# Kernel optimization log

Measured on AMD Instinct MI355X. Metric: run time of the kernel, lower is better.

Reference implementation:

```python
import jax, jax.numpy as jnp
import numpy as np

V, E, H, T, B = 10004, 96, 670, 20, 256


def setup_inputs() -> dict:
    key = jax.random.key(0)
    ks = iter(jax.random.split(key, 48))
    def p(*shape):
        return jax.random.normal(next(ks), shape, jnp.float32) * 0.05
    emb = p(V, E).at[0].set(0.0)  # padding_idx=0 row zeroed
    return dict(
        x=jax.random.randint(next(ks), (B, T), 0, V, jnp.int32),
        emb=emb,
        g_wi=p(4 * H, E), g_wh=p(4 * H, H), g_bi=p(4 * H), g_bh=p(4 * H),
        l_wi=p(4 * H, E), l_wh=p(4 * H, H), l_bi=p(4 * H), l_bh=p(4 * H),
        gl1_w=p(E, H), gl1_b=p(E), ll1_w=p(E, H), ll1_b=p(E),
        gl2_w=p(V, E), gl2_b=p(V), ll2_w=p(V, E), ll2_b=p(V),
        p1_w=p(500, E + 2 * H), p1_b=p(500),
        p2_w=p(250, 500), p2_b=p(250),
        p3_w=p(100, 250), p3_b=p(100),
        p4_w=p(50, 100), p4_b=p(50),
        pe_w=p(2, 50), pe_b=p(2),
        q1_w=p(75, 192), q1_b=p(75),
        q2_w=p(30, 75), q2_b=p(30),
        q2e_w=p(2, 30), q2e_b=p(2),
        q3_w=p(10, 30), q3_b=p(10),
        q3e_w=p(2, 10), q3e_b=p(2),
    )


def _lstm(x, h, c, wi, wh, bi, bh):
    # torch.nn.LSTMCell gate order: i, f, g, o
    g = x @ wi.T + bi + h @ wh.T + bh
    i, f, gg, o = jnp.split(g, 4, axis=-1)
    c = jax.nn.sigmoid(f) * c + jax.nn.sigmoid(i) * jnp.tanh(gg)
    h = jax.nn.sigmoid(o) * jnp.tanh(c)
    return h, c


def reference(x, emb, g_wi, g_wh, g_bi, g_bh, l_wi, l_wh, l_bi, l_bh,
              gl1_w, gl1_b, ll1_w, ll1_b, gl2_w, gl2_b, ll2_w, ll2_b,
              p1_w, p1_b, p2_w, p2_b, p3_w, p3_b, p4_w, p4_b, pe_w, pe_b,
              q1_w, q1_b, q2_w, q2_b, q2e_w, q2e_b, q3_w, q3_b, q3e_w, q3e_b):
    relu = jax.nn.relu
    embs = emb[x]                      # [B,T,E]
    Bb, Tt = x.shape
    Hh = g_wh.shape[1]
    z0 = jnp.zeros((Bb, Hh), embs.dtype)

    def step(carry, e_t):
        gh, gc, lh, lc = carry
        gh, gc = _lstm(e_t, gh, gc, g_wi, g_wh, g_bi, g_bh)
        lh, lc = _lstm(e_t, lh, lc, l_wi, l_wh, l_bi, l_bh)
        h = relu(jnp.concatenate([e_t, gh, lh], 1) @ p1_w.T + p1_b)
        h = relu(h @ p2_w.T + p2_b)
        h = relu(h @ p3_w.T + p3_b)
        h = relu(h @ p4_w.T + p4_b)
        prob = jax.nn.softmax(h @ pe_w.T + pe_b, axis=1)  # [B,2]
        # bmm([B,1,2],[B,2,H]) with tilde=[local, global]
        ghm = prob[:, 0:1] * lh + prob[:, 1:2] * gh
        gcm = prob[:, 0:1] * lc + prob[:, 1:2] * gc
        return (ghm, gcm, lh, lc), (ghm, prob)

    _, (hs, probs) = jax.lax.scan(step, (z0, z0, z0, z0), jnp.swapaxes(embs, 0, 1))
    hidden_states = jnp.swapaxes(hs, 0, 1)    # [B,T,H]
    probs_loop = jnp.swapaxes(probs, 0, 1)    # [B,T,2]

    global_x = hidden_states @ gl1_w.T + gl1_b  # [B,T,E]
    local_x = hidden_states @ ll1_w.T + ll1_b   # [B,T,E]
    sf = jnp.concatenate([global_x, local_x], -1)  # [B,T,192]
    h = relu(sf @ q1_w.T + q1_b)
    h = relu(h @ q2_w.T + q2_b)
    y = relu(h @ q2e_w.T + q2e_b)               # p1 logits [B,T,2]
    h2 = relu(h @ q3_w.T + q3_b)
    zz = relu(h2 @ q3e_w.T + q3e_b)             # p2 logits [B,T,2]

    p1s = jax.nn.softmax(y, axis=2)
    ph = jnp.broadcast_to(probs_loop[:, :, None, :], (Bb, Tt, Tt, 2))  # repeat(1,1,T,1)
    ph = jnp.concatenate([ph, p1s[:, None, :, :]], axis=1)
    xm = p1s[:, :, 0:1] * global_x + p1s[:, :, 1:2] * local_x
    gl = xm @ gl2_w.T + gl2_b                   # [B,T,V]
    ll = xm @ ll2_w.T + ll2_b
    p2s = jax.nn.softmax(zz, axis=2)
    ph = jnp.concatenate([ph, p2s[:, None, :, :]], axis=1)  # [B,T+2,T,2]
    logits = gl * p2s[:, :, 0:1] + ll * p2s[:, :, 1:2]
    return jnp.transpose(logits, (0, 2, 1)), ph
```

## Files before the change

kernel.cpp:

```cpp
#include <hip/hip_runtime.h>

#define DI __device__ __forceinline__

typedef unsigned short u16;
typedef unsigned int u32;
typedef __bf16 bf16x8 __attribute__((ext_vector_type(8)));
typedef float f32x4 __attribute__((ext_vector_type(4)));

static constexpr int B = 256, Tn = 20, En = 96, Hn = 670, Vn = 10004;
static constexpr int HP = 672;

DI float bf2f(u16 u) { union { u32 i; float f; } v; v.i = ((u32)u) << 16; return v.f; }
DI u16 f2bf(float f) {
    u32 u = __float_as_uint(f);
    u32 r = (u + 0x7FFFu + ((u >> 16) & 1u)) >> 16;
    return (u16)r;
}
DI float sigm(float x) { return 1.f / (1.f + __expf(-x)); }
DI float tanha(float x) {
    x = fminf(fmaxf(x, -15.f), 15.f);
    float e = __expf(2.f * x);
    return (e - 1.f) / (e + 1.f);
}
DI bf16x8 frag(const u16* p) { return *(const bf16x8*)p; }
DI f32x4 mfma16(bf16x8 a, bf16x8 b, f32x4 c) {
    return __builtin_amdgcn_mfma_f32_16x16x32_bf16(a, b, c, 0, 0, 0);
}
DI u16 ldw(const u16* src, long long i, int f) {
    return f ? f2bf(((const float*)src)[i]) : src[i];
}
DI float ldf(const u16* src, long long i, int f) {
    return f ? ((const float*)src)[i] : bf2f(src[i]);
}

struct Ptrs {
    const int* x;
    const u16 *emb, *g_wi, *g_wh, *g_bi, *g_bh, *l_wi, *l_wh, *l_bi, *l_bh;
    const u16 *gl1_w, *gl1_b, *ll1_w, *ll1_b, *gl2_w, *gl2_b, *ll2_w, *ll2_b;
    const u16 *p1_w, *p1_b, *p2_w, *p2_b, *p3_w, *p3_b, *p4_w, *p4_b, *pe_w, *pe_b;
    const u16 *q1_w, *q1_b, *q2_w, *q2_b, *q2e_w, *q2e_b, *q3_w, *q3_b, *q3e_w, *q3e_b;
    int  *flagp;
    u16 *embs;
    u16 *WgCat;
    u16 *P1W;
    u16 *W1C;
    u16 *W2C;
    float *BSUM;
    u16 *hs;
    u16 *hcat;
    u16 *uw;
    float *ghf, *gcf, *lhf, *lc2, *gcm;
    float *L1out;
    float *sf;
    float *p2sbuf;
    u16 *n_p1b, *n_p2w, *n_p2b, *n_p3w, *n_p3b, *n_p4w, *n_p4b, *n_pew, *n_peb;
    u16 *n_gl1b, *n_ll1b, *n_gl2b, *n_ll2b;
    u16 *n_q1w, *n_q1b, *n_q2w, *n_q2b, *n_q2ew, *n_q2eb, *n_q3w, *n_q3b, *n_q3ew, *n_q3eb;
    u16 *out0, *out1;
    float *out0f, *out1f;
};

__global__ __launch_bounds__(64) void k_detect(Ptrs p) {
    int lane = threadIdx.x;
    u32 d = ((const u32*)p.g_bi)[lane];
    u16 lo = (u16)(d & 0xffffu);
    int e = (lo >> 7) & 0xff;
    unsigned long long m = __ballot(e >= 127);
    if (lane == 0) p.flagp[0] = (m != 0ull) ? 1 : 0;
}

__global__ __launch_bounds__(256) void k_norm(Ptrs p) {
    const int f = p.flagp[0];
    int i = blockIdx.x * 256 + threadIdx.x;
    const u16* srcs[23] = {p.p1_b, p.p2_w, p.p2_b, p.p3_w, p.p3_b, p.p4_w, p.p4_b,
                           p.pe_w, p.pe_b, p.gl1_b, p.ll1_b, p.gl2_b, p.ll2_b,
                           p.q1_w, p.q1_b, p.q2_w, p.q2_b, p.q2e_w, p.q2e_b,
                           p.q3_w, p.q3_b, p.q3e_w, p.q3e_b};
    u16* dsts[23] = {p.n_p1b, p.n_p2w, p.n_p2b, p.n_p3w, p.n_p3b, p.n_p4w, p.n_p4b,
                     p.n_pew, p.n_peb, p.n_gl1b, p.n_ll1b, p.n_gl2b, p.n_ll2b,
                     p.n_q1w, p.n_q1b, p.n_q2w, p.n_q2b, p.n_q2ew, p.n_q2eb,
                     p.n_q3w, p.n_q3b, p.n_q3ew, p.n_q3eb};
    const int ns[23] = {500, 125000, 250, 25000, 100, 5000, 50, 100, 2, 96, 96, 10004, 10004,
                        14400, 75, 2250, 30, 60, 2, 300, 10, 20, 2};
    #pragma unroll 1
    for (int s = 0; s < 23; ++s) {
        if (i < ns[s]) { dsts[s][i] = ldw(srcs[s], i, f); return; }
        i -= ns[s];
    }
}

__global__ __launch_bounds__(256) void k_prep(Ptrs p) {
    const int f = p.flagp[0];
    int i = blockIdx.x * 256 + threadIdx.x;
    if (i < 491520) {
        int r = i / 96, j = i % 96;
        int t = r >> 8, b = r & 255;
        int idx = p.x[b * Tn + t];
        p.embs[r * 96 + j] = ldw(p.emb, (long long)idx * 96 + j, f);
        return;
    }
    i -= 491520;
    if (i < 2 * 2680 * 768) {
        int z = i / (2680 * 768);
        int rem = i - z * (2680 * 768);
        int col = rem / 768, k = rem % 768;
        const u16* wi = z ? p.l_wi : p.g_wi;
        const u16* wh = z ? p.l_wh : p.g_wh;
        u16 v = 0;
        if (k < 96) v = ldw(wi, col * 96 + k, f);
        else { int j = k - 96; if (j < 670) v = ldw(wh, col * 670 + j, f); }
        p.WgCat[i] = v;
        return;
    }
    i -= 2 * 2680 * 768;
    if (i < 512 * 1440) {
        int col = i / 1440, k = i % 1440;
        u16 v = 0;
        if (col < 500) {
            if (k < 96) v = ldw(p.p1_w, col * 1436 + k, f);
            else if (k < 768) { int j = k - 96;  if (j < 670) v = ldw(p.p1_w, col * 1436 + 96 + j, f); }
            else              { int j = k - 768; if (j < 670) v = ldw(p.p1_w, col * 1436 + 766 + j, f); }
        }
        p.P1W[i] = v;
        return;
    }
    i -= 512 * 1440;
    if (i < 192 * 672) {
        int o = i / 672, h = i % 672;
        u16 v = 0;
        if (h < 670) v = (o < 96) ? ldw(p.gl1_w, o * 670 + h, f) : ldw(p.ll1_w, (o - 96) * 670 + h, f);
        p.W1C[i] = v;
        return;
    }
    i -= 192 * 672;
    if (i < 10112 * 192) {
        int v_ = i / 192, k = i % 192;
        u16 v = 0;
        if (v_ < Vn) v = (k < 96) ? ldw(p.gl2_w, v_ * 96 + k, f) : ldw(p.ll2_w, v_ * 96 + (k - 96), f);
        p.W2C[i] = v;
        return;
    }
    i -= 10112 * 192;
    if (i < 2 * 2680) {
        int z = i / 2680, col = i % 2680;
        const u16* bi = z ? p.l_bi : p.g_bi;
        const u16* bh = z ? p.l_bh : p.g_bh;
        p.BSUM[i] = ldf(bi, col, f) + ldf(bh, col, f);
    }
}

__global__ __launch_bounds__(256) void k_gates(Ptrs p, int t) {
    const int jt = blockIdx.x;
    const int mt = blockIdx.y;
    const int z  = blockIdx.z;
    const int row0 = mt * 32, j0 = jt * 32;
    const int tid = threadIdx.x, lane = tid & 63, wv = tid >> 6;

    __shared__ u16 Al[32 * 40];
    __shared__ u16 Wl[128 * 40];
    __shared__ float bs[128];

    if (tid < 128) {
        int gate = tid >> 5, jj = tid & 31, j = j0 + jj;
        bs[tid] = (j < Hn) ? p.BSUM[z * 2680 + gate * Hn + j] : 0.f;
    }
    const int cur = t & 1, prv = cur ^ 1;
    f32x4 acc[4] = {};
    const int mtw = wv & 1, jh = wv >> 1;

    for (int kc = 0; kc < 24; ++kc) {
        const int kb = kc * 32;
        __syncthreads();
        if (tid < 128) {
            int r = tid >> 2, k8 = (tid & 3) * 8, k = kb + k8;
            int b = row0 + r;
            uint4 val = {0, 0, 0, 0};
            if (k < 96) val = *(const uint4*)&p.embs[(t * 256 + b) * 96 + k];
            else if (t > 0) {
                int kk = k - 96;
                const u16* src = (z == 0) ? (p.hs + (b * Tn + (t - 1)) * HP + kk)
                                          : (p.hcat + prv * (B * 1344) + b * 1344 + 672 + kk);
                val = *(const uint4*)src;
            }
            *(uint4*)&Al[r * 40 + k8] = val;
        }
        #pragma unroll
        for (int it = 0; it < 2; ++it) {
            int idx = tid + it * 256;
            int ri = idx >> 2, k8 = (idx & 3) * 8;
            int gate = ri >> 5, jj = ri & 31, j = j0 + jj;
            uint4 val = {0, 0, 0, 0};
            if (j < Hn) val = *(const uint4*)&p.WgCat[(z * 2680 + gate * Hn + j) * 768 + kb + k8];
            *(uint4*)&Wl[ri * 40 + k8] = val;
        }
        __syncthreads();
        bf16x8 a = frag(&Al[(mtw * 16 + (lane & 15)) * 40 + (lane >> 4) * 8]);
        #pragma unroll
        for (int g = 0; g < 4; ++g) {
            int nt = g * 2 + jh;
            bf16x8 bb = frag(&Wl[(nt * 16 + (lane & 15)) * 40 + (lane >> 4) * 8]);
            acc[g] = mfma16(a, bb, acc[g]);
        }
    }
    const int q = lane >> 4;
    const int jj = jh * 16 + (lane & 15);
    const int j = j0 + jj;
    const bool valid = (j < Hn);
    #pragma unroll
    for (int r = 0; r < 4; ++r) {
        int b = row0 + mtw * 16 + q * 4 + r;
        float I = fminf(fmaxf(acc[0][r] + bs[jj], -30.f), 30.f);
        float F = fminf(fmaxf(acc[1][r] + bs[32 + jj], -30.f), 30.f);
        float G = fminf(fmaxf(acc[2][r] + bs[64 + jj], -30.f), 30.f);
        float O = fminf(fmaxf(acc[3][r] + bs[96 + jj], -30.f), 30.f);
        float cp = 0.f;
        if (valid && t > 0)
            cp = (z == 0) ? p.gcm[b * Hn + j] : p.lc2[prv * (B * Hn) + b * Hn + j];
        float c = sigm(F) * cp + sigm(I) * tanha(G);
        float h = sigm(O) * tanha(c);
        if (z == 0) {
            if (valid) { p.ghf[b * Hn + j] = h; p.gcf[b * Hn + j] = c; }
            p.hcat[cur * (B * 1344) + b * 1344 + j] = valid ? f2bf(h) : (u16)0;
        } else {
            if (valid) { p.lhf[b * Hn + j] = h; p.lc2[cur * (B * Hn) + b * Hn + j] = c; }
            p.hcat[cur * (B * 1344) + b * 1344 + 672 + j] = valid ? f2bf(h) : (u16)0;
        }
    }
}

__global__ __launch_bounds__(256) void k_mlp1(Ptrs p, int t) {
    const int col0 = blockIdx.x * 64;
    const int row0 = blockIdx.y * 32;
    const int tid = threadIdx.x, lane = tid & 63, wv = tid >> 6;
    __shared__ u16 Al[32 * 40];
    __shared__ u16 Wl[64 * 40];
    const int cur = t & 1;
    f32x4 acc[2] = {};
    const int mtw = wv & 1, nh = wv >> 1;
    for (int kc = 0; kc < 45; ++kc) {
        const int kb = kc * 32;
        __syncthreads();
        if (tid < 128) {
            int r = tid >> 2, k8 = (tid & 3) * 8, k = kb + k8;
            int b = row0 + r;
            uint4 val;
            if (k < 96) val = *(const uint4*)&p.embs[(t * 256 + b) * 96 + k];
            else        val = *(const uint4*)&p.hcat[cur * (B * 1344) + b * 1344 + (k - 96)];
            *(uint4*)&Al[r * 40 + k8] = val;
        }
        {
            int ri = tid >> 2, k8 = (tid & 3) * 8;
            *(uint4*)&Wl[ri * 40 + k8] = *(const uint4*)&p.P1W[(col0 + ri) * 1440 + kb + k8];
        }
        __syncthreads();
        bf16x8 a = frag(&Al[(mtw * 16 + (lane & 15)) * 40 + (lane >> 4) * 8]);
        #pragma unroll
        for (int s = 0; s < 2; ++s) {
            int nt = nh + s * 2;
            bf16x8 bb = frag(&Wl[(nt * 16 + (lane & 15)) * 40 + (lane >> 4) * 8]);
            acc[s] = mfma16(a, bb, acc[s]);
        }
    }
    const int q = lane >> 4;
    #pragma unroll
    for (int s = 0; s < 2; ++s) {
        int col = col0 + (nh + s * 2) * 16 + (lane & 15);
        if (col < 500) {
            float bias = bf2f(p.n_p1b[col]);
            #pragma unroll
            for (int r = 0; r < 4; ++r) {
                int b = row0 + mtw * 16 + q * 4 + r;
                p.L1out[b * 500 + col] = fmaxf(acc[s][r] + bias, 0.f);
            }
        }
    }
}

__global__ __launch_bounds__(256) void k_rest(Ptrs p, int t) {
    const int b = blockIdx.x, tid = threadIdx.x;
    const int f = p.flagp[0];
    __shared__ float l1[500];
    __shared__ float h2s[250];
    __shared__ float h3s[100];
    __shared__ float h4s[50];
    __shared__ float pr[2];
    for (int i = tid; i < 125; i += 256)
        *(float4*)&l1[i * 4] = *(const float4*)&p.L1out[b * 500 + i * 4];
    __syncthreads();
    if (tid < 250) {
        const u16* wr = p.n_p2w + tid * 500;
        float s = 0.f;
        for (int k = 0; k < 500; k += 4) {
            uint2 u = *(const uint2*)&wr[k];
            s += l1[k]     * bf2f((u16)(u.x & 0xffff));
            s += l1[k + 1] * bf2f((u16)(u.x >> 16));
            s += l1[k + 2] * bf2f((u16)(u.y & 0xffff));
            s += l1[k + 3] * bf2f((u16)(u.y >> 16));
        }
        h2s[tid] = fmaxf(s + bf2f(p.n_p2b[tid]), 0.f);
    }
    __syncthreads();
    if (tid < 100) {
        const u16* wr = p.n_p3w + tid * 250;
        float s = 0.f;
        for (int k = 0; k < 250; k += 2) {
            u32 u = *(const u32*)&wr[k];
            s += h2s[k]     * bf2f((u16)(u & 0xffff));
            s += h2s[k + 1] * bf2f((u16)(u >> 16));
        }
        h3s[tid] = fmaxf(s + bf2f(p.n_p3b[tid]), 0.f);
    }
    __syncthreads();
    if (tid < 50) {
        const u16* wr = p.n_p4w + tid * 100;
        float s = 0.f;
        for (int k = 0; k < 100; k += 4) {
            uint2 u = *(const uint2*)&wr[k];
            s += h3s[k]     * bf2f((u16)(u.x & 0xffff));
            s += h3s[k + 1] * bf2f((u16)(u.x >> 16));
            s += h3s[k + 2] * bf2f((u16)(u.y & 0xffff));
            s += h3s[k + 3] * bf2f((u16)(u.y >> 16));
        }
        h4s[tid] = fmaxf(s + bf2f(p.n_p4b[tid]), 0.f);
    }
    __syncthreads();
    if (tid == 0) {
        float e0 = bf2f(p.n_peb[0]), e1 = bf2f(p.n_peb[1]);
        for (int k = 0; k < 50; ++k) {
            e0 += h4s[k] * bf2f(p.n_pew[k]);
            e1 += h4s[k] * bf2f(p.n_pew[50 + k]);
        }
        float m = fmaxf(e0, e1);
        float a0 = __expf(e0 - m), a1 = __expf(e1 - m);
        float inv = 1.f / (a0 + a1);
        pr[0] = a0 * inv; pr[1] = a1 * inv;
    }
    __syncthreads();
    float p0 = pr[0], p1 = pr[1];
    const int cur = t & 1;
    for (int j = tid; j < HP; j += 256) {
        u16 hv = 0;
        if (j < Hn) {
            float gm = p0 * p.lhf[b * Hn + j] + p1 * p.ghf[b * Hn + j];
            float cm = p0 * p.lc2[cur * (B * Hn) + b * Hn + j] + p1 * p.gcf[b * Hn + j];
            p.gcm[b * Hn + j] = cm;
            hv = f2bf(gm);
        }
        p.hs[(b * Tn + t) * HP + j] = hv;
    }
    if (tid < 40) {
        long long idx = b * 880 + t * 40 + tid;
        if (f) p.out1f[idx] = pr[tid & 1]; else p.out1[idx] = f2bf(pr[tid & 1]);
    }
}

__global__ __launch_bounds__(256) void k_sf(Ptrs p) {
    const int col0 = blockIdx.x * 64;
    const int row0 = blockIdx.y * 64;
    const int tid = threadIdx.x, lane = tid & 63, wv = tid >> 6;
    __shared__ u16 Al[64 * 40];
    __shared__ u16 Wl[64 * 40];
    f32x4 acc[4] = {};
    for (int kc = 0; kc < 21; ++kc) {
        const int kb = kc * 32;
        __syncthreads();
        {
            int r = tid >> 2, k8 = (tid & 3) * 8;
            *(uint4*)&Al[r * 40 + k8] = *(const uint4*)&p.hs[(row0 + r) * HP + kb + k8];
            *(uint4*)&Wl[r * 40 + k8] = *(const uint4*)&p.W1C[(col0 + r) * HP + kb + k8];
        }
        __syncthreads();
        bf16x8 a = frag(&Al[(wv * 16 + (lane & 15)) * 40 + (lane >> 4) * 8]);
        #pragma unroll
        for (int nt = 0; nt < 4; ++nt) {
            bf16x8 bb = frag(&Wl[(nt * 16 + (lane & 15)) * 40 + (lane >> 4) * 8]);
            acc[nt] = mfma16(a, bb, acc[nt]);
        }
    }
    const int q = lane >> 4;
    #pragma unroll
    for (int nt = 0; nt < 4; ++nt) {
        int col = col0 + nt * 16 + (lane & 15);
        float bias = bf2f(col < 96 ? p.n_gl1b[col] : p.n_ll1b[col - 96]);
        #pragma unroll
        for (int r = 0; r < 4; ++r) {
            int row = row0 + wv * 16 + q * 4 + r;
            p.sf[row * 192 + col] = acc[nt][r] + bias;
        }
    }
}

__global__ __launch_bounds__(256) void k_qchain(Ptrs p) {
    const int b = blockIdx.x, tid = threadIdx.x;
    const int f = p.flagp[0];
    __shared__ float sfl[20 * 192];
    __shared__ float h1[20][80];
    __shared__ float h2[20][32];
    __shared__ float h3[20][12];
    __shared__ float yv[20][2];
    __shared__ float zv[20][2];
    __shared__ float p1s[20][2];
    __shared__ float p2sl[20][2];
    for (int i = tid; i < 960; i += 256)
        *(float4*)&sfl[i * 4] = *(const float4*)&p.sf[b * 3840 + i * 4];
    __syncthreads();
    for (int u = tid; u < 1500; u += 256) {
        int row = u / 75, o = u % 75;
        const u16* wr = p.n_q1w + o * 192;
        const float* sr = &sfl[row * 192];
        float s = bf2f(p.n_q1b[o]);
        for (int k = 0; k < 192; k += 4) {
            uint2 w = *(const uint2*)&wr[k];
            s += sr[k]     * bf2f((u16)(w.x & 0xffff));
            s += sr[k + 1] * bf2f((u16)(w.x >> 16));
            s += sr[k + 2] * bf2f((u16)(w.y & 0xffff));
            s += sr[k + 3] * bf2f((u16)(w.y >> 16));
        }
        h1[row][o] = fmaxf(s, 0.f);
    }
    __syncthreads();
    for (int u = tid; u < 600; u += 256) {
        int row = u / 30, o = u % 30;
        const u16* wr = p.n_q2w + o * 75;
        float s = bf2f(p.n_q2b[o]);
        for (int k = 0; k < 75; ++k) s += h1[row][k] * bf2f(wr[k]);
        h2[row][o] = fmaxf(s, 0.f);
    }
    __syncthreads();
    if (tid < 40) {
        int row = tid >> 1, o = tid & 1;
        const u16* wr = p.n_q2ew + o * 30;
        float s = bf2f(p.n_q2eb[o]);
        for (int k = 0; k < 30; ++k) s += h2[row][k] * bf2f(wr[k]);
        yv[row][o] = fmaxf(s, 0.f);
    } else if (tid >= 56) {
        int u = tid - 56;
        int row = u / 10, o = u % 10;
        const u16* wr = p.n_q3w + o * 30;
        float s = bf2f(p.n_q3b[o]);
        for (int k = 0; k < 30; ++k) s += h2[row][k] * bf2f(wr[k]);
        h3[row][o] = fmaxf(s, 0.f);
    }
    __syncthreads();
    if (tid < 40) {
        int row = tid >> 1, o = tid & 1;
        const u16* wr = p.n_q3ew + o * 10;
        float s = bf2f(p.n_q3eb[o]);
        for (int k = 0; k < 10; ++k) s += h3[row][k] * bf2f(wr[k]);
        zv[row][o] = fmaxf(s, 0.f);
    } else if (tid >= 64 && tid < 84) {
        int row = tid - 64;
        float m = fmaxf(yv[row][0], yv[row][1]);
        float a0 = __expf(yv[row][0] - m), a1 = __expf(yv[row][1] - m);
        float inv = 1.f / (a0 + a1);
        p1s[row][0] = a0 * inv; p1s[row][1] = a1 * inv;
    }
    __syncthreads();
    if (tid < 20) {
        float m = fmaxf(zv[tid][0], zv[tid][1]);
        float a0 = __expf(zv[tid][0] - m), a1 = __expf(zv[tid][1] - m);
        float inv = 1.f / (a0 + a1);
        p2sl[tid][0] = a0 * inv; p2sl[tid][1] = a1 * inv;
        p.p2sbuf[(b * Tn + tid) * 2]     = a0 * inv;
        p.p2sbuf[(b * Tn + tid) * 2 + 1] = a1 * inv;
    } else if (tid >= 64 && tid < 104) {
        int row = (tid - 64) >> 1, c = (tid - 64) & 1;
        long long idx = b * 880 + 800 + row * 2 + c;
        if (f) p.out1f[idx] = p1s[row][c]; else p.out1[idx] = f2bf(p1s[row][c]);
    }
    __syncthreads();
    for (int u = tid; u < 1920; u += 256) {
        int row = u / 96, e = u % 96;
        float xm = p1s[row][0] * sfl[row * 192 + e] + p1s[row][1] * sfl[row * 192 + 96 + e];
        p.uw[(b * Tn + row) * 192 + e]      = f2bf(p2sl[row][0] * xm);
        p.uw[(b * Tn + row) * 192 + 96 + e] = f2bf(p2sl[row][1] * xm);
    }
    if (tid < 40) {
        int row = tid >> 1, c = tid & 1;
        long long idx = b * 880 + 840 + row * 2 + c;
        if (f) p.out1f[idx] = p2sl[row][c]; else p.out1[idx] = f2bf(p2sl[row][c]);
    }
}

__global__ __launch_bounds__(256) void k_final(Ptrs p) {
    const int n0 = blockIdx.x * 64;
    const int v0 = blockIdx.y * 128;
    const int tid = threadIdx.x, lane = tid & 63, wv = tid >> 6;
    const int f = p.flagp[0];
    __shared__ u16 Wl[128 * 104];
    __shared__ u16 Ul[64 * 104];
    f32x4 acc[2][4] = {};
    const int m = lane & 15, q = lane >> 4;
    for (int kc = 0; kc < 2; ++kc) {
        const int kb = kc * 96;
        __syncthreads();
        for (int i = tid; i < 1536; i += 256) {
            int ri = i / 12, k8 = (i % 12) * 8;
            *(uint4*)&Wl[ri * 104 + k8] = *(const uint4*)&p.W2C[(v0 + ri) * 192 + kb + k8];
        }
        for (int i = tid; i < 768; i += 256) {
            int ri = i / 12, k8 = (i % 12) * 8;
            *(uint4*)&Ul[ri * 104 + k8] = *(const uint4*)&p.uw[(n0 + ri) * 192 + kb + k8];
        }
        __syncthreads();
        #pragma unroll
        for (int ks = 0; ks < 3; ++ks) {
            int ko = ks * 32 + q * 8;
            bf16x8 a0 = frag(&Wl[(wv * 32 + m) * 104 + ko]);
            bf16x8 a1 = frag(&Wl[(wv * 32 + 16 + m) * 104 + ko]);
            #pragma unroll
            for (int ni = 0; ni < 4; ++ni) {
                bf16x8 bb = frag(&Ul[(ni * 16 + m) * 104 + ko]);
                acc[0][ni] = mfma16(a0, bb, acc[0][ni]);
                acc[1][ni] = mfma16(a1, bb, acc[1][ni]);
            }
        }
    }
    #pragma unroll
    for (int ni = 0; ni < 4; ++ni) {
        int n = n0 + ni * 16 + m;
        int bb = n / 20, tt = n % 20;
        float s0 = p.p2sbuf[n * 2], s1 = p.p2sbuf[n * 2 + 1];
        size_t base = (size_t)bb * 200080 + tt;
        #pragma unroll
        for (int mi = 0; mi < 2; ++mi) {
            #pragma unroll
            for (int r = 0; r < 4; ++r) {
                int v = v0 + wv * 32 + mi * 16 + q * 4 + r;
                if (v < Vn) {
                    float val = acc[mi][ni][r] + s0 * bf2f(p.n_gl2b[v]) + s1 * bf2f(p.n_ll2b[v]);
                    size_t idx = base + (size_t)v * 20;
                    if (f) p.out0f[idx] = val; else p.out0[idx] = f2bf(val);
                }
            }
        }
    }
}

extern "C" void kernel_launch(void* const* d_in, const int* in_sizes, int n_in,
                              void* d_out, int out_size, void* d_ws, size_t ws_size,
                              hipStream_t stream) {
    Ptrs p;
    p.x    = (const int*)d_in[0];
    p.emb  = (const u16*)d_in[1];
    p.g_wi = (const u16*)d_in[2];  p.g_wh = (const u16*)d_in[3];
    p.g_bi = (const u16*)d_in[4];  p.g_bh = (const u16*)d_in[5];
    p.l_wi = (const u16*)d_in[6];  p.l_wh = (const u16*)d_in[7];
    p.l_bi = (const u16*)d_in[8];  p.l_bh = (const u16*)d_in[9];
    p.gl1_w = (const u16*)d_in[10]; p.gl1_b = (const u16*)d_in[11];
    p.ll1_w = (const u16*)d_in[12]; p.ll1_b = (const u16*)d_in[13];
    p.gl2_w = (const u16*)d_in[14]; p.gl2_b = (const u16*)d_in[15];
    p.ll2_w = (const u16*)d_in[16]; p.ll2_b = (const u16*)d_in[17];
    p.p1_w = (const u16*)d_in[18]; p.p1_b = (const u16*)d_in[19];
    p.p2_w = (const u16*)d_in[20]; p.p2_b = (const u16*)d_in[21];
    p.p3_w = (const u16*)d_in[22]; p.p3_b = (const u16*)d_in[23];
    p.p4_w = (const u16*)d_in[24]; p.p4_b = (const u16*)d_in[25];
    p.pe_w = (const u16*)d_in[26]; p.pe_b = (const u16*)d_in[27];
    p.q1_w = (const u16*)d_in[28]; p.q1_b = (const u16*)d_in[29];
    p.q2_w = (const u16*)d_in[30]; p.q2_b = (const u16*)d_in[31];
    p.q2e_w = (const u16*)d_in[32]; p.q2e_b = (const u16*)d_in[33];
    p.q3_w = (const u16*)d_in[34]; p.q3_b = (const u16*)d_in[35];
    p.q3e_w = (const u16*)d_in[36]; p.q3e_b = (const u16*)d_in[37];

    char* w = (char*)d_ws;
    auto carve = [&](size_t bytes) { char* r = w; w += (bytes + 255) & ~(size_t)255; return r; };
    p.flagp  = (int*)carve(256);
    p.embs   = (u16*)carve((size_t)20 * 256 * 96 * 2);
    p.WgCat  = (u16*)carve((size_t)2 * 2680 * 768 * 2);
    p.P1W    = (u16*)carve((size_t)512 * 1440 * 2);
    p.W1C    = (u16*)carve((size_t)192 * 672 * 2);
    p.W2C    = (u16*)carve((size_t)10112 * 192 * 2);
    p.BSUM   = (float*)carve((size_t)2 * 2680 * 4);
    p.hs     = (u16*)carve((size_t)5120 * 672 * 2);
    p.hcat   = (u16*)carve((size_t)2 * 256 * 1344 * 2);
    p.uw     = (u16*)carve((size_t)5120 * 192 * 2);
    p.ghf    = (float*)carve((size_t)256 * 670 * 4);
    p.gcf    = (float*)carve((size_t)256 * 670 * 4);
    p.lhf    = (float*)carve((size_t)256 * 670 * 4);
    p.lc2    = (float*)carve((size_t)2 * 256 * 670 * 4);
    p.gcm    = (float*)carve((size_t)256 * 670 * 4);
    p.L1out  = (float*)carve((size_t)256 * 500 * 4);
    p.sf     = (float*)carve((size_t)5120 * 192 * 4);
    p.p2sbuf = (float*)carve((size_t)5120 * 2 * 4);
    p.n_p1b = (u16*)carve(500 * 2);   p.n_p2w = (u16*)carve(125000 * 2);
    p.n_p2b = (u16*)carve(250 * 2);   p.n_p3w = (u16*)carve(25000 * 2);
    p.n_p3b = (u16*)carve(100 * 2);   p.n_p4w = (u16*)carve(5000 * 2);
    p.n_p4b = (u16*)carve(50 * 2);    p.n_pew = (u16*)carve(100 * 2);
    p.n_peb = (u16*)carve(2 * 2);
    p.n_gl1b = (u16*)carve(96 * 2);   p.n_ll1b = (u16*)carve(96 * 2);
    p.n_gl2b = (u16*)carve(10004 * 2); p.n_ll2b = (u16*)carve(10004 * 2);
    p.n_q1w = (u16*)carve(14400 * 2); p.n_q1b = (u16*)carve(75 * 2);
    p.n_q2w = (u16*)carve(2250 * 2);  p.n_q2b = (u16*)carve(30 * 2);
    p.n_q2ew = (u16*)carve(60 * 2);   p.n_q2eb = (u16*)carve(2 * 2);
    p.n_q3w = (u16*)carve(300 * 2);   p.n_q3b = (u16*)carve(10 * 2);
    p.n_q3ew = (u16*)carve(20 * 2);   p.n_q3eb = (u16*)carve(2 * 2);
    p.out0 = (u16*)d_out;
    p.out1 = p.out0 + 51220480;
    p.out0f = (float*)d_out;
    p.out1f = p.out0f + 51220480;

    k_detect<<<1, 64, 0, stream>>>(p);
    k_norm<<<756, 256, 0, stream>>>(p);
    k_prep<<<28990, 256, 0, stream>>>(p);
    for (int t = 0; t < 20; ++t) {
        k_gates<<<dim3(21, 8, 2), 256, 0, stream>>>(p, t);
        k_mlp1<<<dim3(8, 8), 256, 0, stream>>>(p, t);
        k_rest<<<256, 256, 0, stream>>>(p, t);
    }
    k_sf<<<dim3(3, 80), 256, 0, stream>>>(p);
    k_qchain<<<256, 256, 0, stream>>>(p);
    k_final<<<dim3(80, 79), 256, 0, stream>>>(p);
}
```

Before: 2.001 ms.

## Fuse recurrent scan into one persistent kernel with grid barriers

The 60 per-timestep launches (gates, mlp1, rest) plus the sf and qchain kernels are replaced by a single persistent kernel of 256 blocks × 512 threads. Each block runs two independent 256-thread jobs that share a shared-memory union, and phases are separated by an atomic-counter grid barrier. This removes kernel launch overhead and the inter-kernel gaps. In exchange it depends on all 256 blocks being co-resident, since otherwise the barrier spins forever, and idle halves still wait at every __syncthreads.

```diff
diff --git a/kernel.cpp b/kernel.cpp
--- a/kernel.cpp
+++ b/kernel.cpp
@@ -39,6 +39,7 @@
     const u16 *gl1_w, *gl1_b, *ll1_w, *ll1_b, *gl2_w, *gl2_b, *ll2_w, *ll2_b;
     const u16 *p1_w, *p1_b, *p2_w, *p2_b, *p3_w, *p3_b, *p4_w, *p4_b, *pe_w, *pe_b;
     const u16 *q1_w, *q1_b, *q2_w, *q2_b, *q2e_w, *q2e_b, *q3_w, *q3_b, *q3e_w, *q3e_b;
+    unsigned *bar;
     int  *flagp;
     u16 *embs;
     u16 *WgCat;
@@ -149,59 +150,68 @@
     }
 }
 
-__global__ __launch_bounds__(256) void k_gates(Ptrs p, int t) {
-    const int jt = blockIdx.x;
-    const int mt = blockIdx.y;
-    const int z  = blockIdx.z;
+struct SA { u16 Al[2][1280]; u16 Wl[2][5120]; float bs[2][128]; };
+struct SB { u16 Al[2][1280]; u16 Wl[2][2560]; };
+struct SC { float l1[2][500]; float h2s[2][250]; float h3s[2][100]; float h4s[2][52]; float pr[2][2]; };
+struct SS { u16 Al[2][2560]; u16 Wl[2][2560]; };
+struct SQ { float sfl[2][3840]; float h1[2][20][80]; float h2[2][20][32]; float h3[2][20][12];
+            float yv[2][20][2]; float zv[2][20][2]; float p1s[2][20][2]; float p2sl[2][20][2]; };
+union SMem { SA a; SB b; SC c; SS s; SQ q; };
+
+DI void phaseA(const Ptrs& p, SA& s, int t, int job, int half, int ht) {
+    const bool act = job < 336;
+    const int jd = act ? job : 0;
+    const int jt = jd % 21;
+    const int r2 = jd / 21;
+    const int mt = r2 & 7, z = r2 >> 3;
     const int row0 = mt * 32, j0 = jt * 32;
-    const int tid = threadIdx.x, lane = tid & 63, wv = tid >> 6;
-
-    __shared__ u16 Al[32 * 40];
-    __shared__ u16 Wl[128 * 40];
-    __shared__ float bs[128];
-
-    if (tid < 128) {
-        int gate = tid >> 5, jj = tid & 31, j = j0 + jj;
-        bs[tid] = (j < Hn) ? p.BSUM[z * 2680 + gate * Hn + j] : 0.f;
+    const int lane = ht & 63, wv = ht >> 6;
+    if (act && ht < 128) {
+        int gate = ht >> 5, jj = ht & 31, j = j0 + jj;
+        s.bs[half][ht] = (j < Hn) ? p.BSUM[z * 2680 + gate * Hn + j] : 0.f;
     }
     const int cur = t & 1, prv = cur ^ 1;
     f32x4 acc[4] = {};
     const int mtw = wv & 1, jh = wv >> 1;
-
     for (int kc = 0; kc < 24; ++kc) {
         const int kb = kc * 32;
         __syncthreads();
-        if (tid < 128) {
-            int r = tid >> 2, k8 = (tid & 3) * 8, k = kb + k8;
-            int b = row0 + r;
-            uint4 val = {0, 0, 0, 0};
-            if (k < 96) val = *(const uint4*)&p.embs[(t * 256 + b) * 96 + k];
-            else if (t > 0) {
-                int kk = k - 96;
-                const u16* src = (z == 0) ? (p.hs + (b * Tn + (t - 1)) * HP + kk)
-                                          : (p.hcat + prv * (B * 1344) + b * 1344 + 672 + kk);
-                val = *(const uint4*)src;
-            }
-            *(uint4*)&Al[r * 40 + k8] = val;
-        }
-        #pragma unroll
-        for (int it = 0; it < 2; ++it) {
-            int idx = tid + it * 256;
-            int ri = idx >> 2, k8 = (idx & 3) * 8;
-            int gate = ri >> 5, jj = ri & 31, j = j0 + jj;
-            uint4 val = {0, 0, 0, 0};
-            if (j < Hn) val = *(const uint4*)&p.WgCat[(z * 2680 + gate * Hn + j) * 768 + kb + k8];
-            *(uint4*)&Wl[ri * 40 + k8] = val;
-        }
-        __syncthreads();
-        bf16x8 a = frag(&Al[(mtw * 16 + (lane & 15)) * 40 + (lane >> 4) * 8]);
-        #pragma unroll
-        for (int g = 0; g < 4; ++g) {
-            int nt = g * 2 + jh;
-            bf16x8 bb = frag(&Wl[(nt * 16 + (lane & 15)) * 40 + (lane >> 4) * 8]);
-            acc[g] = mfma16(a, bb, acc[g]);
-        }
-    }
+        if (act) {
+            if (ht < 128) {
+                int r = ht >> 2, k8 = (ht & 3) * 8, k = kb + k8;
+                int b = row0 + r;
+                uint4 val = {0, 0, 0, 0};
+                if (k < 96) val = *(const uint4*)&p.embs[(t * 256 + b) * 96 + k];
+                else if (t > 0) {
+                    int kk = k - 96;
+                    const u16* src = (z == 0) ? (p.hs + (b * Tn + (t - 1)) * HP + kk)
+                                              : (p.hcat + prv * (B * 1344) + b * 1344 + 672 + kk);
+                    val = *(const uint4*)src;
+                }
+                *(uint4*)&s.Al[half][r * 40 + k8] = val;
+            }
+            #pragma unroll
+            for (int it = 0; it < 2; ++it) {
+                int idx = ht + it * 256;
+                int ri = idx >> 2, k8 = (idx & 3) * 8;
+                int gate = ri >> 5, jj2 = ri & 31, j = j0 + jj2;
+                uint4 val = {0, 0, 0, 0};
+                if (j < Hn) val = *(const uint4*)&p.WgCat[(z * 2680 + gate * Hn + j) * 768 + kb + k8];
+                *(uint4*)&s.Wl[half][ri * 40 + k8] = val;
+            }
+        }
+        __syncthreads();
+        if (act) {
+            bf16x8 a = frag(&s.Al[half][(mtw * 16 + (lane & 15)) * 40 + (lane >> 4) * 8]);
+            #pragma unroll
+            for (int g = 0; g < 4; ++g) {
+                int nt = g * 2 + jh;
+                bf16x8 bb = frag(&s.Wl[half][(nt * 16 + (lane & 15)) * 40 + (lane >> 4) * 8]);
+                acc[g] = mfma16(a, bb, acc[g]);
+            }
+        }
+    }
+    if (!act) return;
     const int q = lane >> 4;
     const int jj = jh * 16 + (lane & 15);
     const int j = j0 + jj;
@@ -209,10 +219,10 @@
     #pragma unroll
     for (int r = 0; r < 4; ++r) {
         int b = row0 + mtw * 16 + q * 4 + r;
-        float I = fminf(fmaxf(acc[0][r] + bs[jj], -30.f), 30.f);
-        float F = fminf(fmaxf(acc[1][r] + bs[32 + jj], -30.f), 30.f);
-        float G = fminf(fmaxf(acc[2][r] + bs[64 + jj], -30.f), 30.f);
-        float O = fminf(fmaxf(acc[3][r] + bs[96 + jj], -30.f), 30.f);
+        float I = fminf(fmaxf(acc[0][r] + s.bs[half][jj], -30.f), 30.f);
+        float F = fminf(fmaxf(acc[1][r] + s.bs[half][32 + jj], -30.f), 30.f);
+        float G = fminf(fmaxf(acc[2][r] + s.bs[half][64 + jj], -30.f), 30.f);
+        float O = fminf(fmaxf(acc[3][r] + s.bs[half][96 + jj], -30.f), 30.f);
         float cp = 0.f;
         if (valid && t > 0)
             cp = (z == 0) ? p.gcm[b * Hn + j] : p.lc2[prv * (B * Hn) + b * Hn + j];
@@ -228,117 +238,120 @@
     }
 }
 
-__global__ __launch_bounds__(256) void k_mlp1(Ptrs p, int t) {
-    const int col0 = blockIdx.x * 64;
-    const int row0 = blockIdx.y * 32;
-    const int tid = threadIdx.x, lane = tid & 63, wv = tid >> 6;
-    __shared__ u16 Al[32 * 40];
-    __shared__ u16 Wl[64 * 40];
+DI void phaseB(const Ptrs& p, SB& s, int t, int job, int half, int ht) {
+    const bool act = job < 64;
+    const int jd = act ? job : 0;
+    const int col0 = (jd & 7) * 64;
+    const int row0 = ((jd >> 3) & 7) * 32;
+    const int lane = ht & 63, wv = ht >> 6;
     const int cur = t & 1;
     f32x4 acc[2] = {};
     const int mtw = wv & 1, nh = wv >> 1;
     for (int kc = 0; kc < 45; ++kc) {
         const int kb = kc * 32;
         __syncthreads();
-        if (tid < 128) {
-            int r = tid >> 2, k8 = (tid & 3) * 8, k = kb + k8;
-            int b = row0 + r;
-            uint4 val;
-            if (k < 96) val = *(const uint4*)&p.embs[(t * 256 + b) * 96 + k];
-            else        val = *(const uint4*)&p.hcat[cur * (B * 1344) + b * 1344 + (k - 96)];
-            *(uint4*)&Al[r * 40 + k8] = val;
-        }
-        {
-            int ri = tid >> 2, k8 = (tid & 3) * 8;
-            *(uint4*)&Wl[ri * 40 + k8] = *(const uint4*)&p.P1W[(col0 + ri) * 1440 + kb + k8];
-        }
-        __syncthreads();
-        bf16x8 a = frag(&Al[(mtw * 16 + (lane & 15)) * 40 + (lane >> 4) * 8]);
-        #pragma unroll
-        for (int s = 0; s < 2; ++s) {
-            int nt = nh + s * 2;
-            bf16x8 bb = frag(&Wl[(nt * 16 + (lane & 15)) * 40 + (lane >> 4) * 8]);
-            acc[s] = mfma16(a, bb, acc[s]);
-        }
-    }
+        if (act) {
+            if (ht < 128) {
+                int r = ht >> 2, k8 = (ht & 3) * 8, k = kb + k8;
+                int b = row0 + r;
+                uint4 val;
+                if (k < 96) val = *(const uint4*)&p.embs[(t * 256 + b) * 96 + k];
+                else        val = *(const uint4*)&p.hcat[cur * (B * 1344) + b * 1344 + (k - 96)];
+                *(uint4*)&s.Al[half][r * 40 + k8] = val;
+            }
+            {
+                int ri = ht >> 2, k8 = (ht & 3) * 8;
+                *(uint4*)&s.Wl[half][ri * 40 + k8] = *(const uint4*)&p.P1W[(col0 + ri) * 1440 + kb + k8];
+            }
+        }
+        __syncthreads();
+        if (act) {
+            bf16x8 a = frag(&s.Al[half][(mtw * 16 + (lane & 15)) * 40 + (lane >> 4) * 8]);
+            #pragma unroll
+            for (int ss = 0; ss < 2; ++ss) {
+                int nt = nh + ss * 2;
+                bf16x8 bb = frag(&s.Wl[half][(nt * 16 + (lane & 15)) * 40 + (lane >> 4) * 8]);
+                acc[ss] = mfma16(a, bb, acc[ss]);
+            }
+        }
+    }
+    if (!act) return;
     const int q = lane >> 4;
     #pragma unroll
-    for (int s = 0; s < 2; ++s) {
-        int col = col0 + (nh + s * 2) * 16 + (lane & 15);
+    for (int ss = 0; ss < 2; ++ss) {
+        int col = col0 + (nh + ss * 2) * 16 + (lane & 15);
         if (col < 500) {
             float bias = bf2f(p.n_p1b[col]);
             #pragma unroll
             for (int r = 0; r < 4; ++r) {
                 int b = row0 + mtw * 16 + q * 4 + r;
-                p.L1out[b * 500 + col] = fmaxf(acc[s][r] + bias, 0.f);
-            }
-        }
-    }
-}
-
-__global__ __launch_bounds__(256) void k_rest(Ptrs p, int t) {
-    const int b = blockIdx.x, tid = threadIdx.x;
-    const int f = p.flagp[0];
-    __shared__ float l1[500];
-    __shared__ float h2s[250];
-    __shared__ float h3s[100];
-    __shared__ float h4s[50];
-    __shared__ float pr[2];
-    for (int i = tid; i < 125; i += 256)
-        *(float4*)&l1[i * 4] = *(const float4*)&p.L1out[b * 500 + i * 4];
-    __syncthreads();
-    if (tid < 250) {
-        const u16* wr = p.n_p2w + tid * 500;
-        float s = 0.f;
+                p.L1out[b * 500 + col] = fmaxf(acc[ss][r] + bias, 0.f);
+            }
+        }
+    }
+}
+
+DI void phaseC(const Ptrs& p, SC& s, int t, int job, int half, int ht, int f) {
+    const bool act = job < 256;
+    const int b = job & 255;
+    if (act) {
+        for (int i = ht; i < 125; i += 256)
+            *(float4*)&s.l1[half][i * 4] = *(const float4*)&p.L1out[b * 500 + i * 4];
+    }
+    __syncthreads();
+    if (act && ht < 250) {
+        const u16* wr = p.n_p2w + ht * 500;
+        float ss = 0.f;
         for (int k = 0; k < 500; k += 4) {
             uint2 u = *(const uint2*)&wr[k];
-            s += l1[k]     * bf2f((u16)(u.x & 0xffff));
-            s += l1[k + 1] * bf2f((u16)(u.x >> 16));
-            s += l1[k + 2] * bf2f((u16)(u.y & 0xffff));
-            s += l1[k + 3] * bf2f((u16)(u.y >> 16));
-        }
-        h2s[tid] = fmaxf(s + bf2f(p.n_p2b[tid]), 0.f);
-    }
-    __syncthreads();
-    if (tid < 100) {
-        const u16* wr = p.n_p3w + tid * 250;
-        float s = 0.f;
+            ss += s.l1[half][k]     * bf2f((u16)(u.x & 0xffff));
+            ss += s.l1[half][k + 1] * bf2f((u16)(u.x >> 16));
+            ss += s.l1[half][k + 2] * bf2f((u16)(u.y & 0xffff));
+            ss += s.l1[half][k + 3] * bf2f((u16)(u.y >> 16));
+        }
+        s.h2s[half][ht] = fmaxf(ss + bf2f(p.n_p2b[ht]), 0.f);
+    }
+    __syncthreads();
+    if (act && ht < 100) {
+        const u16* wr = p.n_p3w + ht * 250;
+        float ss = 0.f;
         for (int k = 0; k < 250; k += 2) {
             u32 u = *(const u32*)&wr[k];
-            s += h2s[k]     * bf2f((u16)(u & 0xffff));
-            s += h2s[k + 1] * bf2f((u16)(u >> 16));
-        }
-        h3s[tid] = fmaxf(s + bf2f(p.n_p3b[tid]), 0.f);
-    }
-    __syncthreads();
-    if (tid < 50) {
-        const u16* wr = p.n_p4w + tid * 100;
-        float s = 0.f;
+            ss += s.h2s[half][k]     * bf2f((u16)(u & 0xffff));
+            ss += s.h2s[half][k + 1] * bf2f((u16)(u >> 16));
+        }
+        s.h3s[half][ht] = fmaxf(ss + bf2f(p.n_p3b[ht]), 0.f);
+    }
+    __syncthreads();
+    if (act && ht < 50) {
+        const u16* wr = p.n_p4w + ht * 100;
+        float ss = 0.f;
         for (int k = 0; k < 100; k += 4) {
             uint2 u = *(const uint2*)&wr[k];
-            s += h3s[k]     * bf2f((u16)(u.x & 0xffff));
-            s += h3s[k + 1] * bf2f((u16)(u.x >> 16));
-            s += h3s[k + 2] * bf2f((u16)(u.y & 0xffff));
-            s += h3s[k + 3] * bf2f((u16)(u.y >> 16));
-        }
-        h4s[tid] = fmaxf(s + bf2f(p.n_p4b[tid]), 0.f);
-    }
-    __syncthreads();
-    if (tid == 0) {
+            ss += s.h3s[half][k]     * bf2f((u16)(u.x & 0xffff));
+            ss += s.h3s[half][k + 1] * bf2f((u16)(u.x >> 16));
+            ss += s.h3s[half][k + 2] * bf2f((u16)(u.y & 0xffff));
+            ss += s.h3s[half][k + 3] * bf2f((u16)(u.y >> 16));
+        }
+        s.h4s[half][ht] = fmaxf(ss + bf2f(p.n_p4b[ht]), 0.f);
+    }
+    __syncthreads();
+    if (act && ht == 0) {
         float e0 = bf2f(p.n_peb[0]), e1 = bf2f(p.n_peb[1]);
         for (int k = 0; k < 50; ++k) {
-            e0 += h4s[k] * bf2f(p.n_pew[k]);
-            e1 += h4s[k] * bf2f(p.n_pew[50 + k]);
+            e0 += s.h4s[half][k] * bf2f(p.n_pew[k]);
+            e1 += s.h4s[half][k] * bf2f(p.n_pew[50 + k]);
         }
         float m = fmaxf(e0, e1);
         float a0 = __expf(e0 - m), a1 = __expf(e1 - m);
         float inv = 1.f / (a0 + a1);
-        pr[0] = a0 * inv; pr[1] = a1 * inv;
-    }
-    __syncthreads();
-    float p0 = pr[0], p1 = pr[1];
+        s.pr[half][0] = a0 * inv; s.pr[half][1] = a1 * inv;
+    }
+    __syncthreads();
+    if (!act) return;
+    float p0 = s.pr[half][0], p1 = s.pr[half][1];
     const int cur = t & 1;
-    for (int j = tid; j < HP; j += 256) {
+    for (int j = ht; j < HP; j += 256) {
         u16 hv = 0;
         if (j < Hn) {
             float gm = p0 * p.lhf[b * Hn + j] + p1 * p.ghf[b * Hn + j];
@@ -348,35 +361,39 @@
         }
         p.hs[(b * Tn + t) * HP + j] = hv;
     }
-    if (tid < 40) {
-        long long idx = b * 880 + t * 40 + tid;
-        if (f) p.out1f[idx] = pr[tid & 1]; else p.out1[idx] = f2bf(pr[tid & 1]);
-    }
-}
-
-__global__ __launch_bounds__(256) void k_sf(Ptrs p) {
-    const int col0 = blockIdx.x * 64;
-    const int row0 = blockIdx.y * 64;
-    const int tid = threadIdx.x, lane = tid & 63, wv = tid >> 6;
-    __shared__ u16 Al[64 * 40];
-    __shared__ u16 Wl[64 * 40];
+    if (ht < 40) {
+        long long idx = b * 880 + t * 40 + ht;
+        float v = (ht & 1) ? p1 : p0;
+        if (f) p.out1f[idx] = v; else p.out1[idx] = f2bf(v);
+    }
+}
+
+DI void phaseSF(const Ptrs& p, SS& s, int job, int half, int ht) {
+    const bool act = job < 240;
+    const int jd = act ? job : 0;
+    const int col0 = (jd % 3) * 64;
+    const int row0 = (jd / 3) * 64;
+    const int lane = ht & 63, wv = ht >> 6;
     f32x4 acc[4] = {};
     for (int kc = 0; kc < 21; ++kc) {
         const int kb = kc * 32;
         __syncthreads();
-        {
-            int r = tid >> 2, k8 = (tid & 3) * 8;
-            *(uint4*)&Al[r * 40 + k8] = *(const uint4*)&p.hs[(row0 + r) * HP + kb + k8];
-            *(uint4*)&Wl[r * 40 + k8] = *(const uint4*)&p.W1C[(col0 + r) * HP + kb + k8];
-        }
-        __syncthreads();
-        bf16x8 a = frag(&Al[(wv * 16 + (lane & 15)) * 40 + (lane >> 4) * 8]);
-        #pragma unroll
-        for (int nt = 0; nt < 4; ++nt) {
-            bf16x8 bb = frag(&Wl[(nt * 16 + (lane & 15)) * 40 + (lane >> 4) * 8]);
-            acc[nt] = mfma16(a, bb, acc[nt]);
-        }
-    }
+        if (act) {
+            int r = ht >> 2, k8 = (ht & 3) * 8;
+            *(uint4*)&s.Al[half][r * 40 + k8] = *(const uint4*)&p.hs[(row0 + r) * HP + kb + k8];
+            *(uint4*)&s.Wl[half][r * 40 + k8] = *(const uint4*)&p.W1C[(col0 + r) * HP + kb + k8];
+        }
+        __syncthreads();
+        if (act) {
+            bf16x8 a = frag(&s.Al[half][(wv * 16 + (lane & 15)) * 40 + (lane >> 4) * 8]);
+            #pragma unroll
+            for (int nt = 0; nt < 4; ++nt) {
+                bf16x8 bb = frag(&s.Wl[half][(nt * 16 + (lane & 15)) * 40 + (lane >> 4) * 8]);
+                acc[nt] = mfma16(a, bb, acc[nt]);
+            }
+        }
+    }
+    if (!act) return;
     const int q = lane >> 4;
     #pragma unroll
     for (int nt = 0; nt < 4; ++nt) {
@@ -390,96 +407,130 @@
     }
 }
 
-__global__ __launch_bounds__(256) void k_qchain(Ptrs p) {
-    const int b = blockIdx.x, tid = threadIdx.x;
-    const int f = p.flagp[0];
-    __shared__ float sfl[20 * 192];
-    __shared__ float h1[20][80];
-    __shared__ float h2[20][32];
-    __shared__ float h3[20][12];
-    __shared__ float yv[20][2];
-    __shared__ float zv[20][2];
-    __shared__ float p1s[20][2];
-    __shared__ float p2sl[20][2];
-    for (int i = tid; i < 960; i += 256)
-        *(float4*)&sfl[i * 4] = *(const float4*)&p.sf[b * 3840 + i * 4];
-    __syncthreads();
-    for (int u = tid; u < 1500; u += 256) {
-        int row = u / 75, o = u % 75;
-        const u16* wr = p.n_q1w + o * 192;
-        const float* sr = &sfl[row * 192];
-        float s = bf2f(p.n_q1b[o]);
-        for (int k = 0; k < 192; k += 4) {
-            uint2 w = *(const uint2*)&wr[k];
-            s += sr[k]     * bf2f((u16)(w.x & 0xffff));
-            s += sr[k + 1] * bf2f((u16)(w.x >> 16));
-            s += sr[k + 2] * bf2f((u16)(w.y & 0xffff));
-            s += sr[k + 3] * bf2f((u16)(w.y >> 16));
-        }
-        h1[row][o] = fmaxf(s, 0.f);
-    }
-    __syncthreads();
-    for (int u = tid; u < 600; u += 256) {
-        int row = u / 30, o = u % 30;
-        const u16* wr = p.n_q2w + o * 75;
-        float s = bf2f(p.n_q2b[o]);
-        for (int k = 0; k < 75; ++k) s += h1[row][k] * bf2f(wr[k]);
-        h2[row][o] = fmaxf(s, 0.f);
-    }
-    __syncthreads();
-    if (tid < 40) {
-        int row = tid >> 1, o = tid & 1;
+DI void phaseQ(const Ptrs& p, SQ& s, int job, int half, int ht, int f) {
+    const bool act = job < 256;
+    const int b = job & 255;
+    if (act) {
+        for (int i = ht; i < 960; i += 256)
+            *(float4*)&s.sfl[half][i * 4] = *(const float4*)&p.sf[b * 3840 + i * 4];
+    }
+    __syncthreads();
+    if (act) {
+        for (int u = ht; u < 1500; u += 256) {
+            int row = u / 75, o = u % 75;
+            const u16* wr = p.n_q1w + o * 192;
+            const float* sr = &s.sfl[half][row * 192];
+            float ss = bf2f(p.n_q1b[o]);
+            for (int k = 0; k < 192; k += 4) {
+                uint2 w = *(const uint2*)&wr[k];
+                ss += sr[k]     * bf2f((u16)(w.x & 0xffff));
+                ss += sr[k + 1] * bf2f((u16)(w.x >> 16));
+                ss += sr[k + 2] * bf2f((u16)(w.y & 0xffff));
+                ss += sr[k + 3] * bf2f((u16)(w.y >> 16));
+            }
+            s.h1[half][row][o] = fmaxf(ss, 0.f);
+        }
+    }
+    __syncthreads();
+    if (act) {
+        for (int u = ht; u < 600; u += 256) {
+            int row = u / 30, o = u % 30;
+            const u16* wr = p.n_q2w + o * 75;
+            float ss = bf2f(p.n_q2b[o]);
+            for (int k = 0; k < 75; ++k) ss += s.h1[half][row][k] * bf2f(wr[k]);
+            s.h2[half][row][o] = fmaxf(ss, 0.f);
+        }
+    }
+    __syncthreads();
+    if (act && ht < 40) {
+        int row = ht >> 1, o = ht & 1;
         const u16* wr = p.n_q2ew + o * 30;
-        float s = bf2f(p.n_q2eb[o]);
-        for (int k = 0; k < 30; ++k) s += h2[row][k] * bf2f(wr[k]);
-        yv[row][o] = fmaxf(s, 0.f);
-    } else if (tid >= 56) {
-        int u = tid - 56;
+        float ss = bf2f(p.n_q2eb[o]);
+        for (int k = 0; k < 30; ++k) ss += s.h2[half][row][k] * bf2f(wr[k]);
+        s.yv[half][row][o] = fmaxf(ss, 0.f);
+    } else if (act && ht >= 56) {
+        int u = ht - 56;
         int row = u / 10, o = u % 10;
         const u16* wr = p.n_q3w + o * 30;
-        float s = bf2f(p.n_q3b[o]);
-        for (int k = 0; k < 30; ++k) s += h2[row][k] * bf2f(wr[k]);
-        h3[row][o] = fmaxf(s, 0.f);
-    }
-    __syncthreads();
-    if (tid < 40) {
-        int row = tid >> 1, o = tid & 1;
+        float ss = bf2f(p.n_q3b[o]);
+        for (int k = 0; k < 30; ++k) ss += s.h2[half][row][k] * bf2f(wr[k]);
+        s.h3[half][row][o] = fmaxf(ss, 0.f);
+    }
+    __syncthreads();
+    if (act && ht < 40) {
+        int row = ht >> 1, o = ht & 1;
         const u16* wr = p.n_q3ew + o * 10;
-        float s = bf2f(p.n_q3eb[o]);
-        for (int k = 0; k < 10; ++k) s += h3[row][k] * bf2f(wr[k]);
-        zv[row][o] = fmaxf(s, 0.f);
-    } else if (tid >= 64 && tid < 84) {
-        int row = tid - 64;
-        float m = fmaxf(yv[row][0], yv[row][1]);
-        float a0 = __expf(yv[row][0] - m), a1 = __expf(yv[row][1] - m);
+        float ss = bf2f(p.n_q3eb[o]);
+        for (int k = 0; k < 10; ++k) ss += s.h3[half][row][k] * bf2f(wr[k]);
+        s.zv[half][row][o] = fmaxf(ss, 0.f);
+    } else if (act && ht >= 64 && ht < 84) {
+        int row = ht - 64;
+        float m = fmaxf(s.yv[half][row][0], s.yv[half][row][1]);
+        float a0 = __expf(s.yv[half][row][0] - m), a1 = __expf(s.yv[half][row][1] - m);
         float inv = 1.f / (a0 + a1);
-        p1s[row][0] = a0 * inv; p1s[row][1] = a1 * inv;
-    }
-    __syncthreads();
-    if (tid < 20) {
-        float m = fmaxf(zv[tid][0], zv[tid][1]);
-        float a0 = __expf(zv[tid][0] - m), a1 = __expf(zv[tid][1] - m);
+        s.p1s[half][row][0] = a0 * inv; s.p1s[half][row][1] = a1 * inv;
+    }
+    __syncthreads();
+    if (act && ht < 20) {
+        float m = fmaxf(s.zv[half][ht][0], s.zv[half][ht][1]);
+        float a0 = __expf(s.zv[half][ht][0] - m), a1 = __expf(s.zv[half][ht][1] - m);
         float inv = 1.f / (a0 + a1);
-        p2sl[tid][0] = a0 * inv; p2sl[tid][1] = a1 * inv;
-        p.p2sbuf[(b * Tn + tid) * 2]     = a0 * inv;
-        p.p2sbuf[(b * Tn + tid) * 2 + 1] = a1 * inv;
-    } else if (tid >= 64 && tid < 104) {
-        int row = (tid - 64) >> 1, c = (tid - 64) & 1;
+        s.p2sl[half][ht][0] = a0 * inv; s.p2sl[half][ht][1] = a1 * inv;
+        p.p2sbuf[(b * Tn + ht) * 2]     = a0 * inv;
+        p.p2sbuf[(b * Tn + ht) * 2 + 1] = a1 * inv;
+    } else if (act && ht >= 64 && ht < 104) {
+        int row = (ht - 64) >> 1, c = (ht - 64) & 1;
         long long idx = b * 880 + 800 + row * 2 + c;
-        if (f) p.out1f[idx] = p1s[row][c]; else p.out1[idx] = f2bf(p1s[row][c]);
-    }
-    __syncthreads();
-    for (int u = tid; u < 1920; u += 256) {
+        if (f) p.out1f[idx] = s.p1s[half][row][c]; else p.out1[idx] = f2bf(s.p1s[half][row][c]);
+    }
+    __syncthreads();
+    if (!act) return;
+    for (int u = ht; u < 1920; u += 256) {
         int row = u / 96, e = u % 96;
-        float xm = p1s[row][0] * sfl[row * 192 + e] + p1s[row][1] * sfl[row * 192 + 96 + e];
-        p.uw[(b * Tn + row) * 192 + e]      = f2bf(p2sl[row][0] * xm);
-        p.uw[(b * Tn + row) * 192 + 96 + e] = f2bf(p2sl[row][1] * xm);
-    }
-    if (tid < 40) {
-        int row = tid >> 1, c = tid & 1;
+        float xm = s.p1s[half][row][0] * s.sfl[half][row * 192 + e]
+                 + s.p1s[half][row][1] * s.sfl[half][row * 192 + 96 + e];
+        p.uw[(b * Tn + row) * 192 + e]      = f2bf(s.p2sl[half][row][0] * xm);
+        p.uw[(b * Tn + row) * 192 + 96 + e] = f2bf(s.p2sl[half][row][1] * xm);
+    }
+    if (ht < 40) {
+        int row = ht >> 1, c = ht & 1;
         long long idx = b * 880 + 840 + row * 2 + c;
-        if (f) p.out1f[idx] = p2sl[row][c]; else p.out1[idx] = f2bf(p2sl[row][c]);
-    }
+        if (f) p.out1f[idx] = s.p2sl[half][row][c]; else p.out1[idx] = f2bf(s.p2sl[half][row][c]);
+    }
+}
+
+#define GSYNC() do {                                                                   \
+    __syncthreads();                                                                   \
+    ++sync_no;                                                                         \
+    if (tid == 0) {                                                                    \
+        __builtin_amdgcn_fence(__ATOMIC_RELEASE, "agent");                             \
+        __hip_atomic_fetch_add(p.bar, 1u, __ATOMIC_RELAXED, __HIP_MEMORY_SCOPE_AGENT); \
+        unsigned tgt = sync_no * 256u;                                                 \
+        while (__hip_atomic_load(p.bar, __ATOMIC_RELAXED, __HIP_MEMORY_SCOPE_AGENT) < tgt) \
+            __builtin_amdgcn_s_sleep(8);                                               \
+        __builtin_amdgcn_fence(__ATOMIC_ACQUIRE, "agent");                             \
+    }                                                                                  \
+    __syncthreads();                                                                   \
+} while (0)
+
+__global__ __launch_bounds__(512, 2) void k_scan(Ptrs p) {
+    __shared__ SMem sm;
+    const int tid = threadIdx.x;
+    const int half = tid >> 8, ht = tid & 255;
+    const int job = blockIdx.x * 2 + half;
+    const int f = p.flagp[0];
+    unsigned sync_no = 0;
+    for (int t = 0; t < Tn; ++t) {
+        phaseA(p, sm.a, t, job, half, ht);
+        GSYNC();
+        phaseB(p, sm.b, t, job, half, ht);
+        GSYNC();
+        phaseC(p, sm.c, t, job, half, ht, f);
+        GSYNC();
+    }
+    phaseSF(p, sm.s, job, half, ht);
+    GSYNC();
+    phaseQ(p, sm.q, job, half, ht, f);
 }
 
 __global__ __launch_bounds__(256) void k_final(Ptrs p) {
@@ -564,6 +615,7 @@
 
     char* w = (char*)d_ws;
     auto carve = [&](size_t bytes) { char* r = w; w += (bytes + 255) & ~(size_t)255; return r; };
+    p.bar    = (unsigned*)carve(256);
     p.flagp  = (int*)carve(256);
     p.embs   = (u16*)carve((size_t)20 * 256 * 96 * 2);
     p.WgCat  = (u16*)carve((size_t)2 * 2680 * 768 * 2);
@@ -599,15 +651,10 @@
     p.out0f = (float*)d_out;
     p.out1f = p.out0f + 51220480;
 
+    hipMemsetAsync(p.bar, 0, 256, stream);
     k_detect<<<1, 64, 0, stream>>>(p);
     k_norm<<<756, 256, 0, stream>>>(p);
     k_prep<<<28990, 256, 0, stream>>>(p);
-    for (int t = 0; t < 20; ++t) {
-        k_gates<<<dim3(21, 8, 2), 256, 0, stream>>>(p, t);
-        k_mlp1<<<dim3(8, 8), 256, 0, stream>>>(p, t);
-        k_rest<<<256, 256, 0, stream>>>(p, t);
-    }
-    k_sf<<<dim3(3, 80), 256, 0, stream>>>(p);
-    k_qchain<<<256, 256, 0, stream>>>(p);
+    k_scan<<<256, 512, 0, stream>>>(p);
     k_final<<<dim3(80, 79), 256, 0, stream>>>(p);
 }
```

Measured after the change: 2.959 ms. 1.48x slower.
